# Kernel optimization log

Measured on AMD Instinct MI355X. Metric: run time of the kernel, lower is better.

The kernel has to match this reference:

```python
import jax, jax.numpy as jnp
import numpy as np

C = 256   # d_model
L = 2     # num_decoder_layers
B = 4
H = 128
W = 128
WH = 8    # dec_win_h
WW = 16   # dec_win_w
EPS = 1e-5


def _gn(x, w, b):
    # GroupNorm with 1 group: normalize over (C,H,W) per sample, per-channel affine
    mu = jnp.mean(x, axis=(1, 2, 3), keepdims=True)
    var = jnp.mean((x - mu) ** 2, axis=(1, 2, 3), keepdims=True)
    xn = (x - mu) * jax.lax.rsqrt(var + EPS)
    return xn * w[:, None, None] + b[:, None, None]


def _conv1x1(x, w, b):
    # x: [B,C,H,W], w: [O,C], b: [O]
    return jnp.einsum('bchw,oc->bohw', x, w) + b[:, None, None]


def _avgpool3(x):
    # AvgPool2d(3, stride=1, padding=1, count_include_pad=False)
    dims = (1, 1, 3, 3)
    strides = (1, 1, 1, 1)
    pad = [(0, 0), (0, 0), (1, 1), (1, 1)]
    s = jax.lax.reduce_window(x, 0.0, jax.lax.add, dims, strides, pad)
    ones = jnp.ones((1, 1) + x.shape[2:], x.dtype)
    cnt = jax.lax.reduce_window(ones, 0.0, jax.lax.add, dims, strides, pad)
    return s / cnt


def _mix(x):
    # PoolFormer token mixer: avgpool(x) - x
    return _avgpool3(x) - x


def _win_part(x, wh, ww):
    # [B,C,H,W] -> [B*nWin, C, wh, ww]
    b, c, h, w = x.shape
    x = x.reshape(b, c, h // wh, wh, w // ww, ww)
    x = x.transpose(0, 2, 4, 1, 3, 5)
    return x.reshape(-1, c, wh, ww)


def _agp(tgt, mem, qw, qb, kw, kb, vw, vb):
    # AttentionGuidedPooling; NOTE: torch uses .view(B,-1,C) on [B,C,H,W],
    # a raw reshape (not a transpose) -- replicated faithfully here.
    bw, c, h, w = mem.shape
    n = h * w
    q = _conv1x1(tgt, qw, qb).reshape(bw, n, c)
    k = _conv1x1(mem, kw, kb).reshape(bw, n, c)
    v = _conv1x1(mem, vw, vb).reshape(bw, n, c)
    attn = jax.nn.softmax(jnp.einsum('bnc,bmc->bnm', q, k), axis=-1)
    out = jnp.einsum('bnm,bmc->bnc', attn, v)
    return out.reshape(bw, c, h, w)


def _layer(tgt, mem, p):
    (gn1_w, gn1_b, gn2_w, gn2_b, ls1, ls2, ls3,
     qw, qb, kw, kb, vw, vb, fc1_w, fc1_b, fc2_w, fc2_b) = p
    tgt2 = tgt + ls1[:, None, None] * _mix(_gn(tgt, gn1_w, gn1_b))
    guided = _agp(tgt, mem, qw, qb, kw, kb, vw, vb)
    tgt3 = tgt2 + guided
    tgt3 = tgt2 + ls2[:, None, None] * _mix(_gn(tgt3, gn1_w, gn1_b))
    h = _gn(tgt3, gn2_w, gn2_b)
    h = _conv1x1(h, fc1_w, fc1_b)
    h = jax.nn.gelu(h, approximate=False)  # torch nn.GELU default (erf)
    h = _conv1x1(h, fc2_w, fc2_b)
    return tgt3 + ls3[:, None, None] * h


def setup_inputs() -> dict:
    key = jax.random.key(0)
    ks = jax.random.split(key, 16)
    s = 0.02
    inp = {
        'src': jax.random.normal(ks[0], (B, C, H, W), jnp.float32),
        'query_feats': jax.random.normal(ks[1], (B, C, H, W), jnp.float32),
        'gn1_w': jnp.ones((L, C), jnp.float32),
        'gn1_b': jnp.zeros((L, C), jnp.float32),
        'gn2_w': jnp.ones((L, C), jnp.float32),
        'gn2_b': jnp.zeros((L, C), jnp.float32),
        'ls1': 1e-5 * jnp.ones((L, C), jnp.float32),
        'ls2': 1e-5 * jnp.ones((L, C), jnp.float32),
        'ls3': 1e-5 * jnp.ones((L, C), jnp.float32),
        'qw': s * jax.random.normal(ks[2], (L, C, C), jnp.float32),
        'qb': jnp.zeros((L, C), jnp.float32),
        'kw': s * jax.random.normal(ks[3], (L, C, C), jnp.float32),
        'kb': jnp.zeros((L, C), jnp.float32),
        'vw': s * jax.random.normal(ks[4], (L, C, C), jnp.float32),
        'vb': jnp.zeros((L, C), jnp.float32),
        'fc1_w': s * jax.random.normal(ks[5], (L, 2 * C, C), jnp.float32),
        'fc1_b': jnp.zeros((L, 2 * C), jnp.float32),
        'fc2_w': s * jax.random.normal(ks[6], (L, C, 2 * C), jnp.float32),
        'fc2_b': jnp.zeros((L, C), jnp.float32),
        'gnf_w': jnp.ones((C,), jnp.float32),
        'gnf_b': jnp.zeros((C,), jnp.float32),
    }
    return inp


def reference(src, query_feats, gn1_w, gn1_b, gn2_w, gn2_b, ls1, ls2, ls3,
              qw, qb, kw, kb, vw, vb, fc1_w, fc1_b, fc2_w, fc2_b, gnf_w, gnf_b):
    # pq_stride=8 -> div_ratio=1: memory windows same size as tgt windows
    mem = _win_part(src, WH, WW)
    out = _win_part(query_feats, WH, WW)
    for l in range(L):
        p = (gn1_w[l], gn1_b[l], gn2_w[l], gn2_b[l], ls1[l], ls2[l], ls3[l],
             qw[l], qb[l], kw[l], kb[l], vw[l], vb[l],
             fc1_w[l], fc1_b[l], fc2_w[l], fc2_b[l])
        out = _layer(out, mem, p)
    out = _gn(out, gnf_w, gnf_b)
    # window reverse -> [B, C, H, W] -> sequence [B, H*W, C]
    nwh, nww = H // WH, W // WW
    x = out.reshape(B, nwh, nww, C, WH, WW).transpose(0, 3, 1, 4, 2, 5)
    x = x.reshape(B, C, H * W)
    hs = jnp.swapaxes(x, 1, 2)[None]        # [1, B, N, C]
    return jnp.swapaxes(hs, 1, 2)           # [1, N, B, C]
```

## Files before the change

kernel.cpp:

```cpp
#include <hip/hip_runtime.h>
#include <hip/hip_bf16.h>

typedef __hip_bfloat16 bf16_t;
typedef short bf16x8 __attribute__((ext_vector_type(8)));
typedef float f32x4 __attribute__((ext_vector_type(4)));

__device__ __forceinline__ float bfr(unsigned short u) {
  return __uint_as_float(((unsigned int)u) << 16);
}
__device__ __forceinline__ float b2f(bf16_t h) { return __bfloat162float(h); }
__device__ __forceinline__ bf16_t f2b(float f) { return __float2bfloat16(f); }
__device__ __forceinline__ unsigned short f2bu(float f) {
  union { bf16_t h; unsigned short u; } cv; cv.h = __float2bfloat16(f); return cv.u;
}
__device__ __forceinline__ void unpk2(unsigned int u, float& a, float& b) {
  a = __uint_as_float(u << 16);
  b = __uint_as_float(u & 0xffff0000u);
}
__device__ __forceinline__ void ld8b(const bf16_t* p, float* o) {
  uint4 v = *(const uint4*)p;
  unpk2(v.x,o[0],o[1]); unpk2(v.y,o[2],o[3]); unpk2(v.z,o[4],o[5]); unpk2(v.w,o[6],o[7]);
}
__device__ __forceinline__ void unpk8(uint4 v, float* o) {
  unpk2(v.x,o[0],o[1]); unpk2(v.y,o[2],o[3]); unpk2(v.z,o[4],o[5]); unpk2(v.w,o[6],o[7]);
}

__global__ void k_flag(const unsigned int* __restrict__ w, int* __restrict__ flg) {
  *flg = (w[0] == 0x3F803F80u) ? 0 : 1;
}

__global__ void k_cvt(const void* __restrict__ s, bf16_t* __restrict__ d, int n,
                      const int* __restrict__ flg) {
  int i = blockIdx.x*256 + threadIdx.x;
  if (i >= n) return;
  d[i] = (*flg) ? f2b(((const float*)s)[i]) : ((const bf16_t*)s)[i];
}

template<int SRC>
__global__ __launch_bounds__(256)
void k_xt(const void* __restrict__ in, bf16_t* __restrict__ out,
          long IW, int IR, int ICbase, int ICt,
          long OW, int OQ, int OCbase, int OCt,
          const int* __restrict__ flg) {
  __shared__ unsigned short L[128*130];
  const int win = blockIdx.x;
  const int tile = blockIdx.y;
  const int tid = threadIdx.x;
  const int IC = ICbase + ICt*tile;
  const int OC = OCbase + OCt*tile;
  const int fl = SRC ? *flg : 0;
  const int b = win >> 7, whi = (win >> 3) & 15, wwi = win & 7;

  for (int i = 0; i < 8; ++i) {
    int idx = tid + i*256;
    int r = idx >> 4, ch = idx & 15;
    unsigned int w0, w1, w2, w3;
    if (SRC) {
      int c = IC + r;
      int hq = ch >> 1, wq = (ch & 1) * 8;
      long gaddr = ((long)((b<<8) + c) << 14) + ((whi<<3) + hq)*128 + (wwi<<4) + wq;
      if (fl) {
        const float* gp = (const float*)in + gaddr;
        float4 a = *(const float4*)gp, bb = *(const float4*)(gp+4);
        w0 = (f2bu(a.y)<<16)|f2bu(a.x); w1 = (f2bu(a.w)<<16)|f2bu(a.z);
        w2 = (f2bu(bb.y)<<16)|f2bu(bb.x); w3 = (f2bu(bb.w)<<16)|f2bu(bb.z);
      } else {
        uint4 v = *(const uint4*)((const bf16_t*)in + gaddr);
        w0 = v.x; w1 = v.y; w2 = v.z; w3 = v.w;
      }
    } else {
      uint4 v = *(const uint4*)((const bf16_t*)in + (long)win*IW + (long)r*IR + IC + ch*8);
      w0 = v.x; w1 = v.y; w2 = v.z; w3 = v.w;
    }
    unsigned int* Lp = (unsigned int*)L;
    int u32o = (r*130 + ch*8) >> 1;
    Lp[u32o+0] = w0; Lp[u32o+1] = w1; Lp[u32o+2] = w2; Lp[u32o+3] = w3;
  }
  __syncthreads();
  for (int i = 0; i < 8; ++i) {
    int idx = tid + i*256;
    int q = idx >> 4, ch = idx & 15;
    unsigned short pk[8];
#pragma unroll
    for (int j = 0; j < 8; ++j) pk[j] = L[(ch*8 + j)*130 + q];
    *(uint4*)(out + (long)win*OW + (long)q*OQ + OC + ch*8) = *(uint4*)pk;
  }
}

__global__ __launch_bounds__(256) void k_statsP(const bf16_t* __restrict__ X, float* __restrict__ st) {
  __shared__ float s1[256], s2[256];
  int w = blockIdx.x, tid = threadIdx.x;
  const bf16_t* x = X + ((long)w << 15);
  float a = 0.f, b = 0.f;
  for (int i = tid*8; i < 32768; i += 2048) {
    float t[8]; ld8b(x + i, t);
#pragma unroll
    for (int j = 0; j < 8; ++j) { a += t[j]; b += t[j]*t[j]; }
  }
  s1[tid] = a; s2[tid] = b;
  __syncthreads();
  for (int off = 128; off > 0; off >>= 1) {
    if (tid < off) { s1[tid] += s1[tid+off]; s2[tid] += s2[tid+off]; }
    __syncthreads();
  }
  if (tid == 0) {
    float mu = s1[0] * (1.0f/32768.0f);
    float var = s2[0] * (1.0f/32768.0f) - mu*mu;
    st[(w<<1)]   = mu;
    st[(w<<1)+1] = rsqrtf(var + 1e-5f);
  }
}

template<int GATH, int STOUT>
__global__ __launch_bounds__(256)
void k_poolf(const bf16_t* __restrict__ Xp, const bf16_t* __restrict__ Gc,
             bf16_t* __restrict__ Out,
             const bf16_t* __restrict__ lsv, const bf16_t* __restrict__ gw,
             float* __restrict__ st_out) {
  __shared__ unsigned short L[32768];
  __shared__ float s1[256], s2[256];
  __shared__ float mr[2];
  const int win = blockIdx.x;
  const int tid = threadIdx.x;
  const long wb = (long)win << 15;
  float a = 0.f, b = 0.f;

#pragma unroll 4
  for (int i = 0; i < 16; ++i) {
    int k = (i<<8) + tid;
    int p = k >> 5, c8 = k & 31;
    uint4 v = *(const uint4*)(Xp + wb + (p<<8) + (c8<<3));
    *(uint4*)&L[(p<<8) + ((c8 ^ (p & 31))<<3)] = v;
    if (!GATH) {
      float t[8]; unpk8(v, t);
#pragma unroll
      for (int j = 0; j < 8; ++j) { a += t[j]; b += t[j]*t[j]; }
    }
  }
  if (GATH) {
    __syncthreads();
#pragma unroll 4
    for (int i = 0; i < 16; ++i) {
      int k = (i<<8) + tid;
      int c = k >> 4, p0 = (k & 15) << 3;
      uint4 gv = *(const uint4*)(Gc + wb + (c<<7) + p0);
      float g[8]; unpk8(gv, g);
      int ch = c >> 3, cl = c & 7;
#pragma unroll
      for (int j = 0; j < 8; ++j) {
        int p = p0 + j;
        int idx = (p<<8) + ((ch ^ (p & 31))<<3) + cl;
        float xx = bfr(L[idx]) + g[j];
        a += xx; b += xx*xx;
        L[idx] = f2bu(xx);
      }
    }
  }
  s1[tid] = a; s2[tid] = b;
  __syncthreads();
  for (int off = 128; off > 0; off >>= 1) {
    if (tid < off) { s1[tid] += s1[tid+off]; s2[tid] += s2[tid+off]; }
    __syncthreads();
  }
  if (tid == 0) {
    float mu = s1[0] * (1.0f/32768.0f);
    float var = s2[0] * (1.0f/32768.0f) - mu*mu;
    mr[0] = mu; mr[1] = rsqrtf(var + 1e-5f);
  }
  __syncthreads();
  const float rstd = mr[1];
  const int c = tid;
  const int ch = c >> 3, cl = c & 7;
  const float scl = b2f(lsv[c]) * b2f(gw[c]) * rstd;
  float oa = 0.f, ob = 0.f;

  float rm1[16], r0[16], rp1[16];
#pragma unroll
  for (int w = 0; w < 16; ++w) {
    int p = w;
    r0[w] = bfr(L[(p<<8) + ((ch ^ (p & 31))<<3) + cl]);
    int p1 = 16 + w;
    rp1[w] = bfr(L[(p1<<8) + ((ch ^ (p1 & 31))<<3) + cl]);
  }
  for (int h = 0; h < 8; ++h) {
    float cs[16];
    float hc = 1.f + (h > 0 ? 1.f : 0.f) + (h < 7 ? 1.f : 0.f);
#pragma unroll
    for (int w = 0; w < 16; ++w)
      cs[w] = r0[w] + (h > 0 ? rm1[w] : 0.f) + (h < 7 ? rp1[w] : 0.f);
#pragma unroll
    for (int w = 0; w < 16; ++w) {
      float s = cs[w];
      float wc = 1.f;
      if (w > 0)  { s += cs[w-1]; wc += 1.f; }
      if (w < 15) { s += cs[w+1]; wc += 1.f; }
      float avg = s / (hc * wc);
      float xx = r0[w];
      int p = (h<<4) + w;
      float base = xx;
      if (GATH) base = bfr(*(const unsigned short*)(Xp + wb + (p<<8) + c));
      float val = base + scl * (avg - xx);
      if (STOUT) { oa += val; ob += val*val; }
      Out[wb + (p<<8) + c] = f2b(val);
    }
#pragma unroll
    for (int w = 0; w < 16; ++w) { rm1[w] = r0[w]; r0[w] = rp1[w]; }
    if (h < 6) {
      int hp = (h+2) << 4;
#pragma unroll
      for (int w = 0; w < 16; ++w) {
        int p = hp + w;
        rp1[w] = bfr(L[(p<<8) + ((ch ^ (p & 31))<<3) + cl]);
      }
    }
  }
  if (STOUT) {
    __syncthreads();
    s1[tid] = oa; s2[tid] = ob;
    __syncthreads();
    for (int off = 128; off > 0; off >>= 1) {
      if (tid < off) { s1[tid] += s1[tid+off]; s2[tid] += s2[tid+off]; }
      __syncthreads();
    }
    if (tid == 0) {
      float mu = s1[0] * (1.0f/32768.0f);
      float var = s2[0] * (1.0f/32768.0f) - mu*mu;
      st_out[(win<<1)]   = mu;
      st_out[(win<<1)+1] = rsqrtf(var + 1e-5f);
    }
  }
}

__global__ void k_gn2(const bf16_t* __restrict__ X, const float* __restrict__ st,
                      const bf16_t* __restrict__ gw, const bf16_t* __restrict__ gb,
                      bf16_t* __restrict__ G) {
  long i8 = ((long)blockIdx.x*256 + threadIdx.x) << 3;
  int win = (int)(i8 >> 15), c0 = (int)(i8 & 255);
  float mu = st[win*2], rs = st[win*2+1];
  float t[8]; ld8b(X + i8, t);
  unsigned short pk[8];
#pragma unroll
  for (int j = 0; j < 8; ++j)
    pk[j] = f2bu((t[j] - mu) * rs * b2f(gw[c0+j]) + b2f(gb[c0+j]));
  *(uint4*)(G + i8) = *(uint4*)pk;
}

template<int OUTM, int EPI>
__global__ __launch_bounds__(256, 2)
void k_gemm_nt(const bf16_t* __restrict__ A, long sA, int lda,
               const bf16_t* __restrict__ Bp, long sB, int ldb,
               bf16_t* __restrict__ Y, long sY, int ldy,
               const bf16_t* __restrict__ bias,
               const bf16_t* __restrict__ res, long sR,
               const bf16_t* __restrict__ ls,
               int K) {
  __shared__ unsigned short As[128*40];
  __shared__ unsigned short Bs[128*40];
  const int win = blockIdx.x;
  const int m0 = blockIdx.y << 7;
  const int tid = threadIdx.x;
  const int w = tid >> 6;
  const int lane = tid & 63;
  const int l15 = lane & 15;
  const int quad = lane >> 4;
  const int m0w = (w >> 1) << 6;
  const int n0w = (w & 1) << 6;
  const bf16_t* Ab = A + (long)win * sA + (long)m0 * lda;
  const bf16_t* Bb = Bp + (long)win * sB;

  f32x4 acc[4][4];
#pragma unroll
  for (int i=0;i<4;++i)
#pragma unroll
    for (int j=0;j<4;++j) acc[i][j] = (f32x4){0.f,0.f,0.f,0.f};

  for (int k0 = 0; k0 < K; k0 += 32) {
#pragma unroll
    for (int i = 0; i < 2; ++i) {
      int idx = tid + (i<<8);
      int r = idx >> 2, ch = idx & 3;
      uint4 va = *(const uint4*)(Ab + (long)r*lda + k0 + (ch<<3));
      *(uint4*)&As[r*40 + (ch<<3)] = va;
      uint4 vb = *(const uint4*)(Bb + (long)r*ldb + k0 + (ch<<3));
      *(uint4*)&Bs[r*40 + (ch<<3)] = vb;
    }
    __syncthreads();
    bf16x8 af[4], bfv[4];
#pragma unroll
    for (int im = 0; im < 4; ++im)
      af[im] = *(const bf16x8*)&As[(m0w + (im<<4) + l15)*40 + (quad<<3)];
#pragma unroll
    for (int in = 0; in < 4; ++in)
      bfv[in] = *(const bf16x8*)&Bs[(n0w + (in<<4) + l15)*40 + (quad<<3)];
#pragma unroll
    for (int im = 0; im < 4; ++im)
#pragma unroll
      for (int in = 0; in < 4; ++in)
        acc[im][in] = __builtin_amdgcn_mfma_f32_16x16x32_bf16(af[im], bfv[in], acc[im][in], 0, 0, 0);
    __syncthreads();
  }

#pragma unroll
  for (int im = 0; im < 4; ++im) {
#pragma unroll
    for (int in = 0; in < 4; ++in) {
      int n = n0w + (in<<4) + l15;
      int mb = m0 + m0w + (im<<4) + (quad<<2);
      f32x4 v = acc[im][in];
      if (OUTM == 0) {
#pragma unroll
        for (int r = 0; r < 4; ++r) {
          int m = mb + r;
          Y[(long)win*sY + (long)m*ldy + n] = f2b(v[r] + b2f(bias[m]));
        }
      } else {
        unsigned short pk[4];
        if (EPI == 0) {
#pragma unroll
          for (int r = 0; r < 4; ++r) pk[r] = f2bu(v[r]);
        } else if (EPI == 2) {
#pragma unroll
          for (int r = 0; r < 4; ++r) {
            float x = v[r] + b2f(bias[mb + r]);
            pk[r] = f2bu(0.5f * x * (1.0f + erff(x * 0.70710678118654752f)));
          }
        } else {
          ushort4 rv = *(const ushort4*)(res + (long)win*sR + (long)n*ldy + mb);
          unsigned short rr[4] = {rv.x, rv.y, rv.z, rv.w};
#pragma unroll
          for (int r = 0; r < 4; ++r) {
            float x = v[r] + b2f(bias[mb + r]);
            pk[r] = f2bu(bfr(rr[r]) + b2f(ls[mb + r]) * x);
          }
        }
        *(ushort4*)(Y + (long)win*sY + (long)n*ldy + mb) = *(ushort4*)pk;
      }
    }
  }
}

__global__ __launch_bounds__(256, 2)
void k_scores(const bf16_t* __restrict__ Kc, const bf16_t* __restrict__ Qc,
              bf16_t* __restrict__ P) {
  __shared__ unsigned short As[128*40];
  __shared__ unsigned short Bs[128*40];
  __shared__ float red[2][2][128];
  const int win = blockIdx.x;
  const int tid = threadIdx.x;
  const int w = tid >> 6;
  const int lane = tid & 63;
  const int l15 = lane & 15;
  const int quad = lane >> 4;
  const int m0w = (w >> 1) << 6;
  const int n0w = (w & 1) << 6;
  const int wrow = w >> 1;
  const bf16_t* Ab = Kc + ((long)win << 15);
  const bf16_t* Bb = Qc + ((long)win << 15);

  f32x4 acc[4][4];
#pragma unroll
  for (int i=0;i<4;++i)
#pragma unroll
    for (int j=0;j<4;++j) acc[i][j] = (f32x4){0.f,0.f,0.f,0.f};

  for (int k0 = 0; k0 < 256; k0 += 32) {
#pragma unroll
    for (int i = 0; i < 2; ++i) {
      int idx = tid + (i<<8);
      int r = idx >> 2, ch = idx & 3;
      *(uint4*)&As[r*40 + (ch<<3)] = *(const uint4*)(Ab + r*256 + k0 + (ch<<3));
      *(uint4*)&Bs[r*40 + (ch<<3)] = *(const uint4*)(Bb + r*256 + k0 + (ch<<3));
    }
    __syncthreads();
    bf16x8 af[4], bfv[4];
#pragma unroll
    for (int im = 0; im < 4; ++im)
      af[im] = *(const bf16x8*)&As[(m0w + (im<<4) + l15)*40 + (quad<<3)];
#pragma unroll
    for (int in = 0; in < 4; ++in)
      bfv[in] = *(const bf16x8*)&Bs[(n0w + (in<<4) + l15)*40 + (quad<<3)];
#pragma unroll
    for (int im = 0; im < 4; ++im)
#pragma unroll
      for (int in = 0; in < 4; ++in)
        acc[im][in] = __builtin_amdgcn_mfma_f32_16x16x32_bf16(af[im], bfv[in], acc[im][in], 0, 0, 0);
    __syncthreads();
  }

  float mx[4];
#pragma unroll
  for (int in = 0; in < 4; ++in) {
    float m = -3.4e38f;
#pragma unroll
    for (int im = 0; im < 4; ++im)
#pragma unroll
      for (int r = 0; r < 4; ++r) m = fmaxf(m, acc[im][in][r]);
    m = fmaxf(m, __shfl_xor(m, 16));
    m = fmaxf(m, __shfl_xor(m, 32));
    mx[in] = m;
  }
  if (quad == 0) {
#pragma unroll
    for (int in = 0; in < 4; ++in) red[0][wrow][n0w + (in<<4) + l15] = mx[in];
  }
  __syncthreads();
  float fm[4];
#pragma unroll
  for (int in = 0; in < 4; ++in) {
    int t = n0w + (in<<4) + l15;
    fm[in] = fmaxf(red[0][0][t], red[0][1][t]);
  }
  float sm[4];
#pragma unroll
  for (int in = 0; in < 4; ++in) {
    float s = 0.f;
#pragma unroll
    for (int im = 0; im < 4; ++im)
#pragma unroll
      for (int r = 0; r < 4; ++r) {
        float e = __expf(acc[im][in][r] - fm[in]);
        acc[im][in][r] = e;
        s += e;
      }
    s += __shfl_xor(s, 16);
    s += __shfl_xor(s, 32);
    sm[in] = s;
  }
  if (quad == 0) {
#pragma unroll
    for (int in = 0; in < 4; ++in) red[1][wrow][n0w + (in<<4) + l15] = sm[in];
  }
  __syncthreads();
  bf16_t* Pw = P + ((long)win << 14);
#pragma unroll
  for (int in = 0; in < 4; ++in) {
    int t = n0w + (in<<4) + l15;
    float inv = 1.0f / (red[1][0][t] + red[1][1][t]);
#pragma unroll
    for (int im = 0; im < 4; ++im) {
      int u = m0w + (im<<4) + (quad<<2);
      unsigned short pk[4];
#pragma unroll
      for (int r = 0; r < 4; ++r) pk[r] = f2bu(acc[im][in][r] * inv);
      *(ushort4*)(Pw + t*128 + u) = *(ushort4*)pk;
    }
  }
}

__global__ void k_final(const bf16_t* __restrict__ Tp, const float* __restrict__ st,
                        const bf16_t* __restrict__ gw, const bf16_t* __restrict__ gb,
                        void* __restrict__ out, const int* __restrict__ flg) {
  const int fl = *flg;
  int idx = blockIdx.x*256 + threadIdx.x;
  int c = idx & 255, p = (idx >> 8) & 127, win = idx >> 15;
  float mu = st[win*2], rs = st[win*2+1];
  float v = (b2f(Tp[idx]) - mu) * rs * b2f(gw[c]) + b2f(gb[c]);
  int b = win >> 7, whi = (win >> 3) & 15, wwi = win & 7;
  int n = ((whi<<3) + (p>>4)) * 128 + (wwi<<4) + (p & 15);
  long o = ((long)((n<<2) + b) << 8) + c;
  if (fl) ((float*)out)[o] = v;
  else    ((bf16_t*)out)[o] = f2b(v);
}

extern "C" void kernel_launch(void* const* d_in, const int* in_sizes, int n_in,
                              void* d_out, int out_size, void* d_ws, size_t ws_size,
                              hipStream_t stream) {
  (void)in_sizes; (void)n_in; (void)out_size; (void)ws_size;
  const void* src   = d_in[0];
  const void* qfeat = d_in[1];

  bf16_t* W    = (bf16_t*)d_ws;
  bf16_t* Tp   = W;
  bf16_t* T2p  = W + 16777216;
  bf16_t* Sp   = W + 33554432;
  bf16_t* slA  = W + 50331648;
  bf16_t* KcGc = W + 67108864;
  bf16_t* Vc   = W + 83886080;
  bf16_t* Hp   = KcGc;
  bf16_t* P    = W + 100663296;
  bf16_t* PR   = W + 109051904;
  float*  ST   = (float*)(W + 110100480);
  float *st0 = ST, *st2 = ST + 2048;
  int* flg = (int*)(ST + 3584);

  bf16_t* gn1w = PR;
  bf16_t* gn2w = PR + 512;
  bf16_t* gn2b = PR + 1024;
  bf16_t* ls1  = PR + 1536;
  bf16_t* ls2  = PR + 2048;
  bf16_t* ls3  = PR + 2560;
  bf16_t* qb   = PR + 3072;
  bf16_t* kb   = PR + 3584;
  bf16_t* vb   = PR + 4096;
  bf16_t* f1b  = PR + 4608;
  bf16_t* f2bp = PR + 5632;
  bf16_t* gfw  = PR + 6144;
  bf16_t* gfb  = PR + 6400;
  bf16_t* qw   = PR + 8192;
  bf16_t* kw   = PR + 139264;
  bf16_t* vw   = PR + 270336;
  bf16_t* f1w  = PR + 401408;
  bf16_t* f2w  = PR + 663552;

  k_flag<<<1, 1, 0, stream>>>((const unsigned int*)d_in[2], flg);

  k_cvt<<<2, 256, 0, stream>>>(d_in[2],  gn1w, 512,    flg);
  k_cvt<<<2, 256, 0, stream>>>(d_in[4],  gn2w, 512,    flg);
  k_cvt<<<2, 256, 0, stream>>>(d_in[5],  gn2b, 512,    flg);
  k_cvt<<<2, 256, 0, stream>>>(d_in[6],  ls1,  512,    flg);
  k_cvt<<<2, 256, 0, stream>>>(d_in[7],  ls2,  512,    flg);
  k_cvt<<<2, 256, 0, stream>>>(d_in[8],  ls3,  512,    flg);
  k_cvt<<<512, 256, 0, stream>>>(d_in[9],  qw, 131072, flg);
  k_cvt<<<2, 256, 0, stream>>>(d_in[10], qb,  512,     flg);
  k_cvt<<<512, 256, 0, stream>>>(d_in[11], kw, 131072, flg);
  k_cvt<<<2, 256, 0, stream>>>(d_in[12], kb,  512,     flg);
  k_cvt<<<512, 256, 0, stream>>>(d_in[13], vw, 131072, flg);
  k_cvt<<<2, 256, 0, stream>>>(d_in[14], vb,  512,     flg);
  k_cvt<<<1024, 256, 0, stream>>>(d_in[15], f1w, 262144, flg);
  k_cvt<<<4, 256, 0, stream>>>(d_in[16], f1b, 1024,    flg);
  k_cvt<<<1024, 256, 0, stream>>>(d_in[17], f2w, 262144, flg);
  k_cvt<<<2, 256, 0, stream>>>(d_in[18], f2bp, 512,    flg);
  k_cvt<<<1, 256, 0, stream>>>(d_in[19], gfw, 256,     flg);
  k_cvt<<<1, 256, 0, stream>>>(d_in[20], gfb, 256,     flg);

  k_xt<1><<<dim3(512,2), 256, 0, stream>>>(qfeat, Tp, 0,0, 0,128, 32768,256, 0,128, flg);
  k_xt<1><<<dim3(512,2), 256, 0, stream>>>(src,   Sp, 0,0, 0,128, 32768,256, 0,128, flg);

  for (int l = 0; l < 2; ++l) {
    k_poolf<0,0><<<512, 256, 0, stream>>>(Tp, nullptr, T2p, ls1 + l*256, gn1w + l*256, nullptr);
    k_gemm_nt<0,1><<<dim3(512,2), 256, 0, stream>>>(
        qw + l*65536, 0, 256, Tp, 32768, 256, slA,  32768, 128, qb + l*256, nullptr, 0, nullptr, 256);
    k_gemm_nt<0,1><<<dim3(512,2), 256, 0, stream>>>(
        kw + l*65536, 0, 256, Sp, 32768, 256, KcGc, 32768, 128, kb + l*256, nullptr, 0, nullptr, 256);
    k_gemm_nt<0,1><<<dim3(512,2), 256, 0, stream>>>(
        vw + l*65536, 0, 256, Sp, 32768, 256, Vc,   32768, 128, vb + l*256, nullptr, 0, nullptr, 256);
    k_scores<<<512, 256, 0, stream>>>(KcGc, slA, P);
    k_xt<0><<<dim3(512,2), 256, 0, stream>>>(Vc, slA, 32768,256, 0,128, 32768,128, 0,16384, flg);
    k_gemm_nt<1,0><<<dim3(512,2), 256, 0, stream>>>(
        slA, 32768, 128, P, 16384, 128, KcGc, 32768, 256, nullptr, nullptr, 0, nullptr, 128);
    k_poolf<1,1><<<512, 256, 0, stream>>>(T2p, KcGc, Tp, ls2 + l*256, gn1w + l*256, st2);
    k_gn2<<<8192, 256, 0, stream>>>(Tp, st2, gn2w + l*256, gn2b + l*256, slA);
    k_gemm_nt<1,2><<<dim3(512,4), 256, 0, stream>>>(
        f1w + l*131072, 0, 256, slA, 32768, 256, Hp, 65536, 512, f1b + l*512, nullptr, 0, nullptr, 256);
    k_gemm_nt<1,3><<<dim3(512,2), 256, 0, stream>>>(
        f2w + l*131072, 0, 512, Hp, 65536, 512, Tp, 32768, 256, f2bp + l*256, Tp, 32768, ls3 + l*256, 512);
  }

  k_statsP<<<512, 256, 0, stream>>>(Tp, st0);
  k_final<<<65536, 256, 0, stream>>>(Tp, st0, gfw, gfb, d_out, flg);
}
```

Measured before the change: 877.0 us.

## Batch QKV GEMMs, fuse GN2 into pool, use direct-to-LDS loads and BK=64

Merges the many per-parameter conversion launches into a single kernel and the two input transposes into one launch. The three Q/K/V projections become one GEMM launch, and the V projection writes its transposed layout directly, which removes the separate transpose kernel. The GroupNorm-2 apply is folded into the second pool kernel through LDS, and all GEMMs switch to global_load_lds with XOR-swizzled 64-wide K tiles. Together these cut launch count and intermediate traffic, at the cost of more complex indexing and no double buffering.

```diff
diff --git a/kernel.cpp b/kernel.cpp
--- a/kernel.cpp
+++ b/kernel.cpp
@@ -24,66 +24,87 @@
 __device__ __forceinline__ void unpk8(uint4 v, float* o) {
   unpk2(v.x,o[0],o[1]); unpk2(v.y,o[2],o[3]); unpk2(v.z,o[4],o[5]); unpk2(v.w,o[6],o[7]);
 }
-
-__global__ void k_flag(const unsigned int* __restrict__ w, int* __restrict__ flg) {
-  *flg = (w[0] == 0x3F803F80u) ? 0 : 1;
-}
-
-__global__ void k_cvt(const void* __restrict__ s, bf16_t* __restrict__ d, int n,
-                      const int* __restrict__ flg) {
-  int i = blockIdx.x*256 + threadIdx.x;
-  if (i >= n) return;
-  d[i] = (*flg) ? f2b(((const float*)s)[i]) : ((const bf16_t*)s)[i];
-}
-
-template<int SRC>
+__device__ __forceinline__ int flag_of(const void* w) {
+  return (*(const unsigned int*)w == 0x3F803F80u) ? 0 : 1;
+}
+
+typedef __attribute__((address_space(3))) void lds_t;
+typedef __attribute__((address_space(1))) void glb_t;
+__device__ __forceinline__ void gll16(const void* g, void* l) {
+  __builtin_amdgcn_global_load_lds((glb_t*)g, (lds_t*)l, 16, 0, 0);
+}
+
+struct Srcs { const void* p[18]; };
+
 __global__ __launch_bounds__(256)
-void k_xt(const void* __restrict__ in, bf16_t* __restrict__ out,
-          long IW, int IR, int ICbase, int ICt,
-          long OW, int OQ, int OCbase, int OCt,
-          const int* __restrict__ flg) {
+void k_cvtall(Srcs a, bf16_t* __restrict__ PR) {
+  const int ck = blockIdx.x*256 + threadIdx.x;
+  if (ck >= 115520) return;
+  constexpr int N8[18]  = {64,64,64,64,64,64,64,64,64,128,64,32,32,16384,16384,16384,32768,32768};
+  constexpr int DOF[18] = {0,512,1024,1536,2048,2560,3072,3584,4096,4608,5632,6144,6400,8192,139264,270336,401408,663552};
+  int s = 0, base = 0, doff = 0, cum = 0;
+#pragma unroll
+  for (int i = 0; i < 17; ++i) {
+    cum += N8[i];
+    if (ck >= cum) { s = i + 1; base = cum; doff = DOF[i + 1]; }
+  }
+  const int o8 = ck - base;
+  const void* sp = a.p[s];
+  const int fl = flag_of(a.p[0]);
+  uint4 w;
+  if (fl) {
+    const float4* f = (const float4*)sp;
+    float4 v0 = f[o8*2], v1 = f[o8*2+1];
+    w.x = ((unsigned)f2bu(v0.y)<<16) | f2bu(v0.x);
+    w.y = ((unsigned)f2bu(v0.w)<<16) | f2bu(v0.z);
+    w.z = ((unsigned)f2bu(v1.y)<<16) | f2bu(v1.x);
+    w.w = ((unsigned)f2bu(v1.w)<<16) | f2bu(v1.z);
+  } else {
+    w = ((const uint4*)sp)[o8];
+  }
+  *(uint4*)(PR + doff + o8*8) = w;
+}
+
+__global__ __launch_bounds__(256)
+void k_xt2(const void* __restrict__ inA, bf16_t* __restrict__ outA,
+           const void* __restrict__ inB, bf16_t* __restrict__ outB,
+           const void* __restrict__ flagw) {
   __shared__ unsigned short L[128*130];
-  const int win = blockIdx.x;
-  const int tile = blockIdx.y;
-  const int tid = threadIdx.x;
-  const int IC = ICbase + ICt*tile;
-  const int OC = OCbase + OCt*tile;
-  const int fl = SRC ? *flg : 0;
+  const void* in = blockIdx.z ? inB : inA;
+  bf16_t* out = blockIdx.z ? outB : outA;
+  const int win = blockIdx.x, tile = blockIdx.y, tid = threadIdx.x;
+  const int IC = tile << 7;
+  const int fl = flag_of(flagw);
   const int b = win >> 7, whi = (win >> 3) & 15, wwi = win & 7;
 
   for (int i = 0; i < 8; ++i) {
-    int idx = tid + i*256;
+    int idx = tid + (i<<8);
     int r = idx >> 4, ch = idx & 15;
     unsigned int w0, w1, w2, w3;
-    if (SRC) {
-      int c = IC + r;
-      int hq = ch >> 1, wq = (ch & 1) * 8;
-      long gaddr = ((long)((b<<8) + c) << 14) + ((whi<<3) + hq)*128 + (wwi<<4) + wq;
-      if (fl) {
-        const float* gp = (const float*)in + gaddr;
-        float4 a = *(const float4*)gp, bb = *(const float4*)(gp+4);
-        w0 = (f2bu(a.y)<<16)|f2bu(a.x); w1 = (f2bu(a.w)<<16)|f2bu(a.z);
-        w2 = (f2bu(bb.y)<<16)|f2bu(bb.x); w3 = (f2bu(bb.w)<<16)|f2bu(bb.z);
-      } else {
-        uint4 v = *(const uint4*)((const bf16_t*)in + gaddr);
-        w0 = v.x; w1 = v.y; w2 = v.z; w3 = v.w;
-      }
+    int c = IC + r;
+    int hq = ch >> 1, wq = (ch & 1) << 3;
+    long gaddr = ((long)((b<<8) + c) << 14) + ((whi<<3) + hq)*128 + (wwi<<4) + wq;
+    if (fl) {
+      const float* gp = (const float*)in + gaddr;
+      float4 aa = *(const float4*)gp, bb = *(const float4*)(gp+4);
+      w0 = ((unsigned)f2bu(aa.y)<<16)|f2bu(aa.x); w1 = ((unsigned)f2bu(aa.w)<<16)|f2bu(aa.z);
+      w2 = ((unsigned)f2bu(bb.y)<<16)|f2bu(bb.x); w3 = ((unsigned)f2bu(bb.w)<<16)|f2bu(bb.z);
     } else {
-      uint4 v = *(const uint4*)((const bf16_t*)in + (long)win*IW + (long)r*IR + IC + ch*8);
+      uint4 v = *(const uint4*)((const bf16_t*)in + gaddr);
       w0 = v.x; w1 = v.y; w2 = v.z; w3 = v.w;
     }
     unsigned int* Lp = (unsigned int*)L;
-    int u32o = (r*130 + ch*8) >> 1;
+    int u32o = (r*130 + (ch<<3)) >> 1;
     Lp[u32o+0] = w0; Lp[u32o+1] = w1; Lp[u32o+2] = w2; Lp[u32o+3] = w3;
   }
   __syncthreads();
   for (int i = 0; i < 8; ++i) {
-    int idx = tid + i*256;
+    int idx = tid + (i<<8);
     int q = idx >> 4, ch = idx & 15;
     unsigned short pk[8];
 #pragma unroll
-    for (int j = 0; j < 8; ++j) pk[j] = L[(ch*8 + j)*130 + q];
-    *(uint4*)(out + (long)win*OW + (long)q*OQ + OC + ch*8) = *(uint4*)pk;
+    for (int j = 0; j < 8; ++j) pk[j] = L[((ch<<3) + j)*130 + q];
+    *(uint4*)(out + (long)win*32768 + (long)q*256 + IC + (ch<<3)) = *(uint4*)pk;
   }
 }
 
@@ -111,12 +132,13 @@
   }
 }
 
-template<int GATH, int STOUT>
+template<int GATH, int GN2>
 __global__ __launch_bounds__(256)
 void k_poolf(const bf16_t* __restrict__ Xp, const bf16_t* __restrict__ Gc,
              bf16_t* __restrict__ Out,
              const bf16_t* __restrict__ lsv, const bf16_t* __restrict__ gw,
-             float* __restrict__ st_out) {
+             bf16_t* __restrict__ G2,
+             const bf16_t* __restrict__ g2w, const bf16_t* __restrict__ g2b) {
   __shared__ unsigned short L[32768];
   __shared__ float s1[256], s2[256];
   __shared__ float mr[2];
@@ -176,45 +198,48 @@
 
   float rm1[16], r0[16], rp1[16];
 #pragma unroll
-  for (int w = 0; w < 16; ++w) {
-    int p = w;
-    r0[w] = bfr(L[(p<<8) + ((ch ^ (p & 31))<<3) + cl]);
-    int p1 = 16 + w;
-    rp1[w] = bfr(L[(p1<<8) + ((ch ^ (p1 & 31))<<3) + cl]);
+  for (int ww = 0; ww < 16; ++ww) {
+    int p = ww;
+    r0[ww] = bfr(L[(p<<8) + ((ch ^ (p & 31))<<3) + cl]);
+    int p1 = 16 + ww;
+    rp1[ww] = bfr(L[(p1<<8) + ((ch ^ (p1 & 31))<<3) + cl]);
   }
   for (int h = 0; h < 8; ++h) {
     float cs[16];
     float hc = 1.f + (h > 0 ? 1.f : 0.f) + (h < 7 ? 1.f : 0.f);
 #pragma unroll
-    for (int w = 0; w < 16; ++w)
-      cs[w] = r0[w] + (h > 0 ? rm1[w] : 0.f) + (h < 7 ? rp1[w] : 0.f);
-#pragma unroll
-    for (int w = 0; w < 16; ++w) {
-      float s = cs[w];
+    for (int ww = 0; ww < 16; ++ww)
+      cs[ww] = r0[ww] + (h > 0 ? rm1[ww] : 0.f) + (h < 7 ? rp1[ww] : 0.f);
+#pragma unroll
+    for (int ww = 0; ww < 16; ++ww) {
+      float s = cs[ww];
       float wc = 1.f;
-      if (w > 0)  { s += cs[w-1]; wc += 1.f; }
-      if (w < 15) { s += cs[w+1]; wc += 1.f; }
+      if (ww > 0)  { s += cs[ww-1]; wc += 1.f; }
+      if (ww < 15) { s += cs[ww+1]; wc += 1.f; }
       float avg = s / (hc * wc);
-      float xx = r0[w];
-      int p = (h<<4) + w;
+      float xx = r0[ww];
+      int p = (h<<4) + ww;
       float base = xx;
       if (GATH) base = bfr(*(const unsigned short*)(Xp + wb + (p<<8) + c));
       float val = base + scl * (avg - xx);
-      if (STOUT) { oa += val; ob += val*val; }
+      if (GN2) {
+        oa += val; ob += val*val;
+        L[(p<<8) + ((ch ^ (p & 31))<<3) + cl] = f2bu(val);
+      }
       Out[wb + (p<<8) + c] = f2b(val);
     }
 #pragma unroll
-    for (int w = 0; w < 16; ++w) { rm1[w] = r0[w]; r0[w] = rp1[w]; }
+    for (int ww = 0; ww < 16; ++ww) { rm1[ww] = r0[ww]; r0[ww] = rp1[ww]; }
     if (h < 6) {
       int hp = (h+2) << 4;
 #pragma unroll
-      for (int w = 0; w < 16; ++w) {
-        int p = hp + w;
-        rp1[w] = bfr(L[(p<<8) + ((ch ^ (p & 31))<<3) + cl]);
-      }
-    }
-  }
-  if (STOUT) {
+      for (int ww = 0; ww < 16; ++ww) {
+        int p = hp + ww;
+        rp1[ww] = bfr(L[(p<<8) + ((ch ^ (p & 31))<<3) + cl]);
+      }
+    }
+  }
+  if (GN2) {
     __syncthreads();
     s1[tid] = oa; s2[tid] = ob;
     __syncthreads();
@@ -225,165 +250,287 @@
     if (tid == 0) {
       float mu = s1[0] * (1.0f/32768.0f);
       float var = s2[0] * (1.0f/32768.0f) - mu*mu;
-      st_out[(win<<1)]   = mu;
-      st_out[(win<<1)+1] = rsqrtf(var + 1e-5f);
-    }
-  }
-}
-
-__global__ void k_gn2(const bf16_t* __restrict__ X, const float* __restrict__ st,
-                      const bf16_t* __restrict__ gw, const bf16_t* __restrict__ gb,
-                      bf16_t* __restrict__ G) {
-  long i8 = ((long)blockIdx.x*256 + threadIdx.x) << 3;
-  int win = (int)(i8 >> 15), c0 = (int)(i8 & 255);
-  float mu = st[win*2], rs = st[win*2+1];
-  float t[8]; ld8b(X + i8, t);
-  unsigned short pk[8];
-#pragma unroll
-  for (int j = 0; j < 8; ++j)
-    pk[j] = f2bu((t[j] - mu) * rs * b2f(gw[c0+j]) + b2f(gb[c0+j]));
-  *(uint4*)(G + i8) = *(uint4*)pk;
-}
-
-template<int OUTM, int EPI>
+      mr[0] = mu; mr[1] = rsqrtf(var + 1e-5f);
+    }
+    __syncthreads();
+    const float mu2 = mr[0], rs2 = mr[1];
+#pragma unroll 4
+    for (int i = 0; i < 16; ++i) {
+      int k = (i<<8) + tid;
+      int p = k >> 5, cv = k & 31;
+      uint4 v = *(const uint4*)&L[(p<<8) + ((cv ^ (p & 31))<<3)];
+      float t[8]; unpk8(v, t);
+      uint4 wv = *(const uint4*)(g2w + (cv<<3));
+      uint4 bv = *(const uint4*)(g2b + (cv<<3));
+      float wf[8], bf2[8]; unpk8(wv, wf); unpk8(bv, bf2);
+      unsigned short pk[8];
+#pragma unroll
+      for (int j = 0; j < 8; ++j) pk[j] = f2bu((t[j]-mu2)*rs2*wf[j] + bf2[j]);
+      *(uint4*)(G2 + wb + (p<<8) + (cv<<3)) = *(uint4*)pk;
+    }
+  }
+}
+
+#define GM_QKV  0
+#define GM_NM   1
+#define GM_GELU 2
+#define GM_RES  3
+
+template<int MODE>
 __global__ __launch_bounds__(256, 2)
-void k_gemm_nt(const bf16_t* __restrict__ A, long sA, int lda,
-               const bf16_t* __restrict__ Bp, long sB, int ldb,
-               bf16_t* __restrict__ Y, long sY, int ldy,
-               const bf16_t* __restrict__ bias,
-               const bf16_t* __restrict__ res, long sR,
-               const bf16_t* __restrict__ ls,
-               int K) {
-  __shared__ unsigned short As[128*40];
-  __shared__ unsigned short Bs[128*40];
+void k_gemm(const bf16_t* __restrict__ A, long sA, int lda,
+            const bf16_t* __restrict__ B0, const bf16_t* __restrict__ B1,
+            long sB, int ldb,
+            bf16_t* __restrict__ Y, long sY, int ldy,
+            const bf16_t* __restrict__ bias,
+            const bf16_t* __restrict__ res, long sR,
+            const bf16_t* __restrict__ ls,
+            int K) {
+  __shared__ uint4 LB[2048];
+  unsigned short* As = (unsigned short*)LB;
+  unsigned short* Bs = (unsigned short*)LB + 8192;
+  unsigned short* E  = (unsigned short*)LB;
   const int win = blockIdx.x;
-  const int m0 = blockIdx.y << 7;
   const int tid = threadIdx.x;
-  const int w = tid >> 6;
-  const int lane = tid & 63;
-  const int l15 = lane & 15;
-  const int quad = lane >> 4;
-  const int m0w = (w >> 1) << 6;
-  const int n0w = (w & 1) << 6;
-  const bf16_t* Ab = A + (long)win * sA + (long)m0 * lda;
-  const bf16_t* Bb = Bp + (long)win * sB;
+  const int w = tid >> 6, lane = tid & 63;
+  const int l15 = lane & 15, quad = lane >> 4;
+  const int m0w = (w >> 1) << 6, n0w = (w & 1) << 6;
+
+  int sel = 0, m0;
+  const bf16_t *Ab, *Bb; bf16_t* Yb; const bf16_t* biasb = nullptr;
+  if (MODE == GM_QKV) {
+    sel = blockIdx.y >> 1; m0 = (blockIdx.y & 1) << 7;
+    Ab = A + sel*131072 + (long)m0*lda;
+    Bb = (sel ? B1 : B0) + (long)win*sB;
+    Yb = Y + (long)sel*16777216 + (long)win*sY;
+    biasb = bias + sel*512 + m0;
+  } else {
+    m0 = blockIdx.y << 7;
+    Ab = A + (long)win*sA + (long)m0*lda;
+    Bb = B0 + (long)win*sB;
+    Yb = Y + (long)win*sY;
+    if (bias) biasb = bias + m0;
+  }
+  const bool CT = (MODE == GM_QKV) && (sel < 2);
+
+  int rr_[4], co_[4], lo_[4];
+#pragma unroll
+  for (int j = 0; j < 4; ++j) {
+    int ck = (j<<8) + (w<<6) + lane;
+    int r = ck >> 3;
+    rr_[j] = r;
+    co_[j] = ((ck & 7) ^ (r & 7)) << 3;
+    lo_[j] = ((j<<8) + (w<<6)) << 3;
+  }
 
   f32x4 acc[4][4];
 #pragma unroll
-  for (int i=0;i<4;++i)
-#pragma unroll
-    for (int j=0;j<4;++j) acc[i][j] = (f32x4){0.f,0.f,0.f,0.f};
-
-  for (int k0 = 0; k0 < K; k0 += 32) {
-#pragma unroll
-    for (int i = 0; i < 2; ++i) {
-      int idx = tid + (i<<8);
-      int r = idx >> 2, ch = idx & 3;
-      uint4 va = *(const uint4*)(Ab + (long)r*lda + k0 + (ch<<3));
-      *(uint4*)&As[r*40 + (ch<<3)] = va;
-      uint4 vb = *(const uint4*)(Bb + (long)r*ldb + k0 + (ch<<3));
-      *(uint4*)&Bs[r*40 + (ch<<3)] = vb;
-    }
-    __syncthreads();
-    bf16x8 af[4], bfv[4];
-#pragma unroll
-    for (int im = 0; im < 4; ++im)
-      af[im] = *(const bf16x8*)&As[(m0w + (im<<4) + l15)*40 + (quad<<3)];
-#pragma unroll
-    for (int in = 0; in < 4; ++in)
-      bfv[in] = *(const bf16x8*)&Bs[(n0w + (in<<4) + l15)*40 + (quad<<3)];
-#pragma unroll
-    for (int im = 0; im < 4; ++im)
-#pragma unroll
-      for (int in = 0; in < 4; ++in)
-        acc[im][in] = __builtin_amdgcn_mfma_f32_16x16x32_bf16(af[im], bfv[in], acc[im][in], 0, 0, 0);
-    __syncthreads();
-  }
-
-#pragma unroll
-  for (int im = 0; im < 4; ++im) {
-#pragma unroll
-    for (int in = 0; in < 4; ++in) {
-      int n = n0w + (in<<4) + l15;
-      int mb = m0 + m0w + (im<<4) + (quad<<2);
-      f32x4 v = acc[im][in];
-      if (OUTM == 0) {
-#pragma unroll
-        for (int r = 0; r < 4; ++r) {
-          int m = mb + r;
-          Y[(long)win*sY + (long)m*ldy + n] = f2b(v[r] + b2f(bias[m]));
-        }
+  for (int i = 0; i < 4; ++i)
+#pragma unroll
+    for (int j = 0; j < 4; ++j) acc[i][j] = (f32x4){0.f,0.f,0.f,0.f};
+
+  for (int k0 = 0; k0 < K; k0 += 64) {
+#pragma unroll
+    for (int j = 0; j < 4; ++j) {
+      gll16(Ab + (long)rr_[j]*lda + k0 + co_[j], As + lo_[j]);
+      gll16(Bb + (long)rr_[j]*ldb + k0 + co_[j], Bs + lo_[j]);
+    }
+    __syncthreads();
+#pragma unroll
+    for (int kk = 0; kk < 2; ++kk) {
+      bf16x8 af[4], bv[4];
+#pragma unroll
+      for (int im = 0; im < 4; ++im) {
+        int R = m0w + (im<<4) + l15;
+        af[im] = *(const bf16x8*)&As[(R<<6) + ((((kk<<2)+quad) ^ (R&7))<<3)];
+      }
+#pragma unroll
+      for (int in = 0; in < 4; ++in) {
+        int R = n0w + (in<<4) + l15;
+        bv[in] = *(const bf16x8*)&Bs[(R<<6) + ((((kk<<2)+quad) ^ (R&7))<<3)];
+      }
+      if (CT) {
+#pragma unroll
+        for (int im = 0; im < 4; ++im)
+#pragma unroll
+          for (int in = 0; in < 4; ++in)
+            acc[im][in] = __builtin_amdgcn_mfma_f32_16x16x32_bf16(bv[in], af[im], acc[im][in], 0, 0, 0);
       } else {
-        unsigned short pk[4];
-        if (EPI == 0) {
-#pragma unroll
-          for (int r = 0; r < 4; ++r) pk[r] = f2bu(v[r]);
-        } else if (EPI == 2) {
-#pragma unroll
-          for (int r = 0; r < 4; ++r) {
-            float x = v[r] + b2f(bias[mb + r]);
-            pk[r] = f2bu(0.5f * x * (1.0f + erff(x * 0.70710678118654752f)));
-          }
-        } else {
-          ushort4 rv = *(const ushort4*)(res + (long)win*sR + (long)n*ldy + mb);
-          unsigned short rr[4] = {rv.x, rv.y, rv.z, rv.w};
-#pragma unroll
-          for (int r = 0; r < 4; ++r) {
-            float x = v[r] + b2f(bias[mb + r]);
-            pk[r] = f2bu(bfr(rr[r]) + b2f(ls[mb + r]) * x);
+#pragma unroll
+        for (int im = 0; im < 4; ++im)
+#pragma unroll
+          for (int in = 0; in < 4; ++in)
+            acc[im][in] = __builtin_amdgcn_mfma_f32_16x16x32_bf16(af[im], bv[in], acc[im][in], 0, 0, 0);
+      }
+    }
+    __syncthreads();
+  }
+
+  if (MODE == GM_QKV && sel == 2) {
+#pragma unroll
+    for (int im = 0; im < 4; ++im) {
+#pragma unroll
+      for (int in = 0; in < 4; ++in) {
+        f32x4 v = acc[im][in];
+        int tok = n0w + (in<<4) + l15;
+        int c0 = m0w + (im<<4) + (quad<<2);
+        int u0 = c0 >> 1;
+        float x0 = v[0] + b2f(biasb[c0]);
+        float x1 = v[1] + b2f(biasb[c0+1]);
+        float x2 = v[2] + b2f(biasb[c0+2]);
+        float x3 = v[3] + b2f(biasb[c0+3]);
+        int sl = (((u0>>3) ^ (tok&7))<<3) + (u0&7);
+        *(unsigned int*)&E[(tok<<6) + sl]       = (unsigned)f2bu(x0) | ((unsigned)f2bu(x2)<<16);
+        *(unsigned int*)&E[((128+tok)<<6) + sl] = (unsigned)f2bu(x1) | ((unsigned)f2bu(x3)<<16);
+      }
+    }
+    __syncthreads();
+#pragma unroll
+    for (int i = 0; i < 8; ++i) {
+      int ck = (i<<8) + tid;
+      int cp = ck >> 3, u8 = ck & 7;
+      uint4 v = *(const uint4*)&E[(cp<<6) + ((u8 ^ (cp&7))<<3)];
+      *(uint4*)(Yb + (long)cp*128 + (m0>>1) + (u8<<3)) = v;
+    }
+    return;
+  }
+
+  if (CT) {
+#pragma unroll
+    for (int half = 0; half < 2; ++half) {
+      if (m0w == (half<<6)) {
+#pragma unroll
+        for (int im = 0; im < 4; ++im) {
+          int row = (im<<4) + l15;
+          float bm = b2f(biasb[(half<<6) + row]);
+#pragma unroll
+          for (int in = 0; in < 4; ++in) {
+            f32x4 v = acc[im][in];
+            unsigned short pk[4];
+#pragma unroll
+            for (int r = 0; r < 4; ++r) pk[r] = f2bu(v[r] + bm);
+            *(ushort4*)&E[row*136 + n0w + (in<<4) + (quad<<2)] = *(ushort4*)pk;
           }
         }
-        *(ushort4*)(Y + (long)win*sY + (long)n*ldy + mb) = *(ushort4*)pk;
-      }
-    }
+      }
+      __syncthreads();
+#pragma unroll
+      for (int i = 0; i < 4; ++i) {
+        int ck = (i<<8) + tid;
+        int row = ck >> 4, c8 = (ck & 15) << 3;
+        uint4 v = *(const uint4*)&E[row*136 + c8];
+        *(uint4*)(Yb + (long)(m0 + (half<<6) + row)*ldy + c8) = v;
+      }
+      __syncthreads();
+    }
+    return;
+  }
+
+#pragma unroll
+  for (int half = 0; half < 2; ++half) {
+    if (n0w == (half<<6)) {
+#pragma unroll
+      for (int in = 0; in < 4; ++in) {
+        int row = (in<<4) + l15;
+#pragma unroll
+        for (int im = 0; im < 4; ++im) {
+          f32x4 v = acc[im][in];
+          int mb = m0w + (im<<4) + (quad<<2);
+          unsigned short pk[4];
+#pragma unroll
+          for (int r = 0; r < 4; ++r) {
+            float x = v[r];
+            if (MODE == GM_GELU || MODE == GM_RES) x += b2f(biasb[mb + r]);
+            if (MODE == GM_GELU) x = 0.5f * x * (1.0f + erff(x * 0.70710678118654752f));
+            pk[r] = f2bu(x);
+          }
+          *(ushort4*)&E[row*136 + mb] = *(ushort4*)pk;
+        }
+      }
+    }
+    __syncthreads();
+#pragma unroll
+    for (int i = 0; i < 4; ++i) {
+      int ck = (i<<8) + tid;
+      int rloc = ck >> 4, c8 = (ck & 15) << 3;
+      long oadr = (long)((half<<6) + rloc)*ldy + m0 + c8;
+      uint4 v = *(const uint4*)&E[rloc*136 + c8];
+      if (MODE == GM_RES) {
+        float t[8]; unpk8(v, t);
+        uint4 rv = *(const uint4*)(res + (long)win*sR + oadr);
+        float rf[8]; unpk8(rv, rf);
+        uint4 lv = *(const uint4*)(ls + m0 + c8);
+        float lf[8]; unpk8(lv, lf);
+        unsigned short pk[8];
+#pragma unroll
+        for (int j = 0; j < 8; ++j) pk[j] = f2bu(rf[j] + lf[j]*t[j]);
+        *(uint4*)(Yb + oadr) = *(uint4*)pk;
+      } else {
+        *(uint4*)(Yb + oadr) = v;
+      }
+    }
+    __syncthreads();
   }
 }
 
 __global__ __launch_bounds__(256, 2)
 void k_scores(const bf16_t* __restrict__ Kc, const bf16_t* __restrict__ Qc,
               bf16_t* __restrict__ P) {
-  __shared__ unsigned short As[128*40];
-  __shared__ unsigned short Bs[128*40];
+  __shared__ uint4 LB[2048];
   __shared__ float red[2][2][128];
+  unsigned short* As = (unsigned short*)LB;
+  unsigned short* Bs = (unsigned short*)LB + 8192;
   const int win = blockIdx.x;
   const int tid = threadIdx.x;
-  const int w = tid >> 6;
-  const int lane = tid & 63;
-  const int l15 = lane & 15;
-  const int quad = lane >> 4;
-  const int m0w = (w >> 1) << 6;
-  const int n0w = (w & 1) << 6;
+  const int w = tid >> 6, lane = tid & 63;
+  const int l15 = lane & 15, quad = lane >> 4;
+  const int m0w = (w >> 1) << 6, n0w = (w & 1) << 6;
   const int wrow = w >> 1;
   const bf16_t* Ab = Kc + ((long)win << 15);
   const bf16_t* Bb = Qc + ((long)win << 15);
 
+  int rr_[4], co_[4], lo_[4];
+#pragma unroll
+  for (int j = 0; j < 4; ++j) {
+    int ck = (j<<8) + (w<<6) + lane;
+    int r = ck >> 3;
+    rr_[j] = r;
+    co_[j] = ((ck & 7) ^ (r & 7)) << 3;
+    lo_[j] = ((j<<8) + (w<<6)) << 3;
+  }
+
   f32x4 acc[4][4];
 #pragma unroll
-  for (int i=0;i<4;++i)
-#pragma unroll
-    for (int j=0;j<4;++j) acc[i][j] = (f32x4){0.f,0.f,0.f,0.f};
-
-  for (int k0 = 0; k0 < 256; k0 += 32) {
-#pragma unroll
-    for (int i = 0; i < 2; ++i) {
-      int idx = tid + (i<<8);
-      int r = idx >> 2, ch = idx & 3;
-      *(uint4*)&As[r*40 + (ch<<3)] = *(const uint4*)(Ab + r*256 + k0 + (ch<<3));
-      *(uint4*)&Bs[r*40 + (ch<<3)] = *(const uint4*)(Bb + r*256 + k0 + (ch<<3));
-    }
-    __syncthreads();
-    bf16x8 af[4], bfv[4];
-#pragma unroll
-    for (int im = 0; im < 4; ++im)
-      af[im] = *(const bf16x8*)&As[(m0w + (im<<4) + l15)*40 + (quad<<3)];
-#pragma unroll
-    for (int in = 0; in < 4; ++in)
-      bfv[in] = *(const bf16x8*)&Bs[(n0w + (in<<4) + l15)*40 + (quad<<3)];
-#pragma unroll
-    for (int im = 0; im < 4; ++im)
-#pragma unroll
-      for (int in = 0; in < 4; ++in)
-        acc[im][in] = __builtin_amdgcn_mfma_f32_16x16x32_bf16(af[im], bfv[in], acc[im][in], 0, 0, 0);
+  for (int i = 0; i < 4; ++i)
+#pragma unroll
+    for (int j = 0; j < 4; ++j) acc[i][j] = (f32x4){0.f,0.f,0.f,0.f};
+
+  for (int k0 = 0; k0 < 256; k0 += 64) {
+#pragma unroll
+    for (int j = 0; j < 4; ++j) {
+      gll16(Ab + (long)rr_[j]*256 + k0 + co_[j], As + lo_[j]);
+      gll16(Bb + (long)rr_[j]*256 + k0 + co_[j], Bs + lo_[j]);
+    }
+    __syncthreads();
+#pragma unroll
+    for (int kk = 0; kk < 2; ++kk) {
+      bf16x8 af[4], bv[4];
+#pragma unroll
+      for (int im = 0; im < 4; ++im) {
+        int R = m0w + (im<<4) + l15;
+        af[im] = *(const bf16x8*)&As[(R<<6) + ((((kk<<2)+quad) ^ (R&7))<<3)];
+      }
+#pragma unroll
+      for (int in = 0; in < 4; ++in) {
+        int R = n0w + (in<<4) + l15;
+        bv[in] = *(const bf16x8*)&Bs[(R<<6) + ((((kk<<2)+quad) ^ (R&7))<<3)];
+      }
+#pragma unroll
+      for (int im = 0; im < 4; ++im)
+#pragma unroll
+        for (int in = 0; in < 4; ++in)
+          acc[im][in] = __builtin_amdgcn_mfma_f32_16x16x32_bf16(af[im], bv[in], acc[im][in], 0, 0, 0);
+    }
     __syncthreads();
   }
 
@@ -449,8 +596,8 @@
 
 __global__ void k_final(const bf16_t* __restrict__ Tp, const float* __restrict__ st,
                         const bf16_t* __restrict__ gw, const bf16_t* __restrict__ gb,
-                        void* __restrict__ out, const int* __restrict__ flg) {
-  const int fl = *flg;
+                        void* __restrict__ out, const void* __restrict__ flagw) {
+  const int fl = flag_of(flagw);
   int idx = blockIdx.x*256 + threadIdx.x;
   int c = idx & 255, p = (idx >> 8) & 127, win = idx >> 15;
   float mu = st[win*2], rs = st[win*2+1];
@@ -480,8 +627,7 @@
   bf16_t* P    = W + 100663296;
   bf16_t* PR   = W + 109051904;
   float*  ST   = (float*)(W + 110100480);
-  float *st0 = ST, *st2 = ST + 2048;
-  int* flg = (int*)(ST + 3584);
+  float*  st0  = ST;
 
   bf16_t* gn1w = PR;
   bf16_t* gn2w = PR + 512;
@@ -490,62 +636,41 @@
   bf16_t* ls2  = PR + 2048;
   bf16_t* ls3  = PR + 2560;
   bf16_t* qb   = PR + 3072;
-  bf16_t* kb   = PR + 3584;
-  bf16_t* vb   = PR + 4096;
   bf16_t* f1b  = PR + 4608;
   bf16_t* f2bp = PR + 5632;
   bf16_t* gfw  = PR + 6144;
   bf16_t* gfb  = PR + 6400;
   bf16_t* qw   = PR + 8192;
-  bf16_t* kw   = PR + 139264;
-  bf16_t* vw   = PR + 270336;
   bf16_t* f1w  = PR + 401408;
   bf16_t* f2w  = PR + 663552;
 
-  k_flag<<<1, 1, 0, stream>>>((const unsigned int*)d_in[2], flg);
-
-  k_cvt<<<2, 256, 0, stream>>>(d_in[2],  gn1w, 512,    flg);
-  k_cvt<<<2, 256, 0, stream>>>(d_in[4],  gn2w, 512,    flg);
-  k_cvt<<<2, 256, 0, stream>>>(d_in[5],  gn2b, 512,    flg);
-  k_cvt<<<2, 256, 0, stream>>>(d_in[6],  ls1,  512,    flg);
-  k_cvt<<<2, 256, 0, stream>>>(d_in[7],  ls2,  512,    flg);
-  k_cvt<<<2, 256, 0, stream>>>(d_in[8],  ls3,  512,    flg);
-  k_cvt<<<512, 256, 0, stream>>>(d_in[9],  qw, 131072, flg);
-  k_cvt<<<2, 256, 0, stream>>>(d_in[10], qb,  512,     flg);
-  k_cvt<<<512, 256, 0, stream>>>(d_in[11], kw, 131072, flg);
-  k_cvt<<<2, 256, 0, stream>>>(d_in[12], kb,  512,     flg);
-  k_cvt<<<512, 256, 0, stream>>>(d_in[13], vw, 131072, flg);
-  k_cvt<<<2, 256, 0, stream>>>(d_in[14], vb,  512,     flg);
-  k_cvt<<<1024, 256, 0, stream>>>(d_in[15], f1w, 262144, flg);
-  k_cvt<<<4, 256, 0, stream>>>(d_in[16], f1b, 1024,    flg);
-  k_cvt<<<1024, 256, 0, stream>>>(d_in[17], f2w, 262144, flg);
-  k_cvt<<<2, 256, 0, stream>>>(d_in[18], f2bp, 512,    flg);
-  k_cvt<<<1, 256, 0, stream>>>(d_in[19], gfw, 256,     flg);
-  k_cvt<<<1, 256, 0, stream>>>(d_in[20], gfb, 256,     flg);
-
-  k_xt<1><<<dim3(512,2), 256, 0, stream>>>(qfeat, Tp, 0,0, 0,128, 32768,256, 0,128, flg);
-  k_xt<1><<<dim3(512,2), 256, 0, stream>>>(src,   Sp, 0,0, 0,128, 32768,256, 0,128, flg);
+  Srcs sa;
+  const int map[18] = {2,4,5,6,7,8,10,12,14,16,18,19,20,9,11,13,15,17};
+  for (int i = 0; i < 18; ++i) sa.p[i] = d_in[map[i]];
+  k_cvtall<<<452, 256, 0, stream>>>(sa, PR);
+
+  k_xt2<<<dim3(512,2,2), 256, 0, stream>>>(qfeat, Tp, src, Sp, d_in[2]);
 
   for (int l = 0; l < 2; ++l) {
-    k_poolf<0,0><<<512, 256, 0, stream>>>(Tp, nullptr, T2p, ls1 + l*256, gn1w + l*256, nullptr);
-    k_gemm_nt<0,1><<<dim3(512,2), 256, 0, stream>>>(
-        qw + l*65536, 0, 256, Tp, 32768, 256, slA,  32768, 128, qb + l*256, nullptr, 0, nullptr, 256);
-    k_gemm_nt<0,1><<<dim3(512,2), 256, 0, stream>>>(
-        kw + l*65536, 0, 256, Sp, 32768, 256, KcGc, 32768, 128, kb + l*256, nullptr, 0, nullptr, 256);
-    k_gemm_nt<0,1><<<dim3(512,2), 256, 0, stream>>>(
-        vw + l*65536, 0, 256, Sp, 32768, 256, Vc,   32768, 128, vb + l*256, nullptr, 0, nullptr, 256);
+    k_poolf<0,0><<<512, 256, 0, stream>>>(Tp, nullptr, T2p, ls1 + l*256, gn1w + l*256,
+                                          nullptr, nullptr, nullptr);
+    k_gemm<GM_QKV><<<dim3(512,6), 256, 0, stream>>>(
+        qw + l*65536, 0, 256, Tp, Sp, 32768, 256, slA, 32768, 128,
+        qb + l*256, nullptr, 0, nullptr, 256);
     k_scores<<<512, 256, 0, stream>>>(KcGc, slA, P);
-    k_xt<0><<<dim3(512,2), 256, 0, stream>>>(Vc, slA, 32768,256, 0,128, 32768,128, 0,16384, flg);
-    k_gemm_nt<1,0><<<dim3(512,2), 256, 0, stream>>>(
-        slA, 32768, 128, P, 16384, 128, KcGc, 32768, 256, nullptr, nullptr, 0, nullptr, 128);
-    k_poolf<1,1><<<512, 256, 0, stream>>>(T2p, KcGc, Tp, ls2 + l*256, gn1w + l*256, st2);
-    k_gn2<<<8192, 256, 0, stream>>>(Tp, st2, gn2w + l*256, gn2b + l*256, slA);
-    k_gemm_nt<1,2><<<dim3(512,4), 256, 0, stream>>>(
-        f1w + l*131072, 0, 256, slA, 32768, 256, Hp, 65536, 512, f1b + l*512, nullptr, 0, nullptr, 256);
-    k_gemm_nt<1,3><<<dim3(512,2), 256, 0, stream>>>(
-        f2w + l*131072, 0, 512, Hp, 65536, 512, Tp, 32768, 256, f2bp + l*256, Tp, 32768, ls3 + l*256, 512);
+    k_gemm<GM_NM><<<dim3(512,2), 256, 0, stream>>>(
+        Vc, 32768, 128, P, nullptr, 16384, 128, KcGc, 32768, 256,
+        nullptr, nullptr, 0, nullptr, 128);
+    k_poolf<1,1><<<512, 256, 0, stream>>>(T2p, KcGc, Tp, ls2 + l*256, gn1w + l*256,
+                                          slA, gn2w + l*256, gn2b + l*256);
+    k_gemm<GM_GELU><<<dim3(512,4), 256, 0, stream>>>(
+        f1w + l*131072, 0, 256, slA, nullptr, 32768, 256, Hp, 65536, 512,
+        f1b + l*512, nullptr, 0, nullptr, 256);
+    k_gemm<GM_RES><<<dim3(512,2), 256, 0, stream>>>(
+        f2w + l*131072, 0, 512, Hp, nullptr, 65536, 512, Tp, 32768, 256,
+        f2bp + l*256, Tp, 32768, ls3 + l*256, 512);
   }
 
   k_statsP<<<512, 256, 0, stream>>>(Tp, st0);
-  k_final<<<65536, 256, 0, stream>>>(Tp, st0, gfw, gfb, d_out, flg);
-}
+  k_final<<<65536, 256, 0, stream>>>(Tp, st0, gfw, gfb, d_out, d_in[2]);
+}
```

After: 817.0 us. 1.07x faster.
